# Performance work log

Measured on AMD Instinct MI355X. Metric: run time of the kernel, lower is better.

The kernel has to match this reference:

```python
import jax, jax.numpy as jnp
import numpy as np

N_NODES = 100000
N_EDGES = 600000
NODE_IN = 387
HID = 128
EDGE_DIM = 7


def _p(key, shape, scale=0.02):
    return jax.random.normal(key, shape, dtype=jnp.float32) * scale


def setup_inputs() -> dict:
    key = jax.random.key(0)
    ks = jax.random.split(key, 24)
    x = jax.random.normal(ks[0], (N_NODES, NODE_IN), dtype=jnp.float32)
    edge_index = jax.random.randint(ks[1], (2, N_EDGES), 0, N_NODES, dtype=jnp.int64)
    edge_attr = jax.random.normal(ks[2], (N_EDGES, EDGE_DIM), dtype=jnp.float32)
    return {
        "x": x,
        "edge_index": edge_index,
        "edge_attr": edge_attr,
        # conv1: edge lin (7 -> 387), mlp (387 -> 128 -> 128)
        "e1_w": _p(ks[3], (EDGE_DIM, NODE_IN)), "e1_b": jnp.zeros((NODE_IN,), jnp.float32),
        "m1_w1": _p(ks[4], (NODE_IN, HID)), "m1_b1": jnp.zeros((HID,), jnp.float32),
        "m1_w2": _p(ks[5], (HID, HID)), "m1_b2": jnp.zeros((HID,), jnp.float32),
        # conv2: edge lin (7 -> 128), mlp (128 -> 128 -> 128)
        "e2_w": _p(ks[6], (EDGE_DIM, HID)), "e2_b": jnp.zeros((HID,), jnp.float32),
        "m2_w1": _p(ks[7], (HID, HID)), "m2_b1": jnp.zeros((HID,), jnp.float32),
        "m2_w2": _p(ks[8], (HID, HID)), "m2_b2": jnp.zeros((HID,), jnp.float32),
        # edge_mlp: (2*128+7 -> 128 -> 2); dropout is identity at eval
        "em_w1": _p(ks[9], (2 * HID + EDGE_DIM, HID)), "em_b1": jnp.zeros((HID,), jnp.float32),
        "em_w2": _p(ks[10], (HID, 2)), "em_b2": jnp.zeros((2,), jnp.float32),
    }


def gine_conv(x, src, dst, edge_attr, ew, eb, w1, b1, w2, b2, eps=0.0):
    # message: relu(x_j + Lin(edge_attr)); aggregate sum at destination
    msg = jax.nn.relu(x[src] + edge_attr @ ew + eb)  # [E, D]
    aggr = jax.ops.segment_sum(msg, dst, num_segments=x.shape[0])  # [N, D]
    h = (1.0 + eps) * x + aggr
    return jax.nn.relu(h @ w1 + b1) @ w2 + b2


def reference(x, edge_index, edge_attr,
              e1_w, e1_b, m1_w1, m1_b1, m1_w2, m1_b2,
              e2_w, e2_b, m2_w1, m2_b1, m2_w2, m2_b2,
              em_w1, em_b1, em_w2, em_b2):
    src, dst = edge_index[0], edge_index[1]
    h = gine_conv(x, src, dst, edge_attr, e1_w, e1_b, m1_w1, m1_b1, m1_w2, m1_b2)
    h = jax.nn.relu(h)
    h = gine_conv(h, src, dst, edge_attr, e2_w, e2_b, m2_w1, m2_b1, m2_w2, m2_b2)
    h = jax.nn.relu(h)
    edge_input = jnp.concatenate([h[src], h[dst], edge_attr], axis=1)  # [E, 263]
    return jax.nn.relu(edge_input @ em_w1 + em_b1) @ em_w2 + em_b2  # [E, 2]
```

## Files before the change

kernel.cpp:

```cpp
#include <hip/hip_runtime.h>


using f32x4 = __attribute__((ext_vector_type(4))) float;
using s16x8 = __attribute__((ext_vector_type(8))) short;

#define N_NODES 100000
#define N_EDGES 600000
#define NODE_IN 387
#define KPAD    416
#define HID     128
#define NB_SCAN 391

__device__ __forceinline__ unsigned short f2bf(float f) {
    unsigned u = __float_as_uint(f);
    u += 0x7FFFu + ((u >> 16) & 1u);
    return (unsigned short)(u >> 16);
}

__global__ __launch_bounds__(256) void k_decode(const unsigned* __restrict__ w,
                                                int* __restrict__ s32,
                                                int* __restrict__ d32) {
    __shared__ unsigned long long bs[4];
    __shared__ int is64_s;
    const int t = threadIdx.x;
    unsigned any = 0;
    for (int i = 1 + 2 * t; i < 2048; i += 512) any |= w[i];
    unsigned long long b = __ballot(any != 0);
    if ((t & 63) == 0) bs[t >> 6] = b;
    __syncthreads();
    if (t == 0) is64_s = ((bs[0] | bs[1] | bs[2] | bs[3]) == 0ULL) ? 1 : 0;
    __syncthreads();
    const int is64 = is64_s;
    const int e = blockIdx.x * 256 + t;
    if (e < N_EDGES) {
        if (is64) {
            s32[e] = (int)w[2 * e];
            d32[e] = (int)w[2 * N_EDGES + 2 * e];
        } else {
            s32[e] = (int)w[e];
            d32[e] = (int)w[N_EDGES + e];
        }
    }
}

__global__ __launch_bounds__(256) void k_prep(const float* __restrict__ w1,
                                              const float* __restrict__ w2,
                                              const float* __restrict__ v1,
                                              const float* __restrict__ v2,
                                              const float* __restrict__ ew1,
                                              unsigned short* __restrict__ W1t,
                                              unsigned short* __restrict__ W2t,
                                              unsigned short* __restrict__ V1t,
                                              unsigned short* __restrict__ V2t,
                                              unsigned short* __restrict__ EW1t) {
    int i = blockIdx.x * 256 + threadIdx.x;
    if (i < 128 * KPAD) {
        int c = i / KPAD, k = i - c * KPAD;
        W1t[i] = (k < NODE_IN) ? f2bf(w1[k * HID + c]) : (unsigned short)0;
        return;
    }
    i -= 128 * KPAD;
    if (i < 16384) { int c = i >> 7, k = i & 127; W2t[i] = f2bf(w2[k * HID + c]); return; }
    i -= 16384;
    if (i < 16384) { int c = i >> 7, k = i & 127; V1t[i] = f2bf(v1[k * HID + c]); return; }
    i -= 16384;
    if (i < 16384) { int c = i >> 7, k = i & 127; V2t[i] = f2bf(v2[k * HID + c]); return; }
    i -= 16384;
    if (i < 32768) { int c = i >> 8, k = i & 255; EW1t[i] = f2bf(ew1[k * HID + c]); return; }
}

__global__ __launch_bounds__(256) void k_hist(const int* __restrict__ d32,
                                              int* __restrict__ cnt) {
    const int e = blockIdx.x * 256 + threadIdx.x;
    if (e < N_EDGES) atomicAdd(&cnt[d32[e]], 1);
}

__global__ __launch_bounds__(256) void k_scanA(const int* __restrict__ cnt,
                                               int* __restrict__ bsum) {
    __shared__ int wt[4];
    const int t = threadIdx.x;
    const int i = blockIdx.x * 256 + t;
    int v = (i < N_NODES) ? cnt[i] : 0;
#pragma unroll
    for (int off = 32; off; off >>= 1) v += __shfl_down(v, off);
    if ((t & 63) == 0) wt[t >> 6] = v;
    __syncthreads();
    if (t == 0) bsum[blockIdx.x] = wt[0] + wt[1] + wt[2] + wt[3];
}

__global__ __launch_bounds__(256) void k_scanC(int* __restrict__ cnt,
                                               const int* __restrict__ bsum) {
    __shared__ int wt[4];
    __shared__ int wt2[4];
    __shared__ int sh_bofs;
    const int t = threadIdx.x, b = blockIdx.x;
    int accp = 0;
    for (int i = t; i < NB_SCAN; i += 256) if (i < b) accp += bsum[i];
#pragma unroll
    for (int off = 32; off; off >>= 1) accp += __shfl_down(accp, off);
    if ((t & 63) == 0) wt[t >> 6] = accp;
    __syncthreads();
    if (t == 0) sh_bofs = wt[0] + wt[1] + wt[2] + wt[3];
    const int i = b * 256 + t;
    const int v = (i < N_NODES) ? cnt[i] : 0;
    int inc = v;
    const int lane = t & 63;
#pragma unroll
    for (int off = 1; off < 64; off <<= 1) {
        int u = __shfl_up(inc, off);
        if (lane >= off) inc += u;
    }
    if (lane == 63) wt2[t >> 6] = inc;
    __syncthreads();
    int wbase = 0;
    for (int wI = 0; wI < (t >> 6); ++wI) wbase += wt2[wI];
    if (i < N_NODES) cnt[i] = sh_bofs + wbase + inc - v;
}

__global__ __launch_bounds__(256) void k_scatter(const int* __restrict__ s32,
                                                 const int* __restrict__ d32,
                                                 int* __restrict__ cur,
                                                 int* __restrict__ ss2,
                                                 int* __restrict__ ds2,
                                                 int* __restrict__ ep) {
    const int e = blockIdx.x * 256 + threadIdx.x;
    if (e < N_EDGES) {
        const int d = d32[e];
        const int pos = atomicAdd(&cur[d], 1);
        ss2[pos] = s32[e];
        ds2[pos] = d;
        ep[pos]  = e;
    }
}

#define STAGE_B(dst, srcbase, stride_) do {                                   \
    const int col_ = t >> 1, h_ = t & 1;                                      \
    *(s16x8*)&(dst)[col_ * 40 + h_ * 16] =                                    \
        *(const s16x8*)&(srcbase)[col_ * (stride_) + h_ * 16];                \
    *(s16x8*)&(dst)[col_ * 40 + h_ * 16 + 8] =                                \
        *(const s16x8*)&(srcbase)[col_ * (stride_) + h_ * 16 + 8];            \
} while (0)

__global__ __launch_bounds__(256) void k_edge1(const float* __restrict__ x,
                                               const int* __restrict__ ss2,
                                               const int* __restrict__ ds2,
                                               const int* __restrict__ ep,
                                               const float* __restrict__ ea,
                                               const float* __restrict__ e1w,
                                               const float* __restrict__ e1b,
                                               const unsigned short* __restrict__ W1t,
                                               float* __restrict__ yagg) {
    __shared__ __align__(16) char pool[31488];
    unsigned short* Asm = (unsigned short*)(pool);
    unsigned short* Bsm = (unsigned short*)(pool + 5120);
    float* e1w_s = (float*)(pool + 15360);
    float* e1b_s = (float*)(pool + 27008);
    float* ea_s  = (float*)(pool + 28672);
    int* ss_s    = (int*)(pool + 30720);
    int* dst_s   = (int*)(pool + 30976);
    int* ep_s    = (int*)(pool + 31232);
    float* Csm   = (float*)(pool);

    const int t = threadIdx.x;
    const int e0 = blockIdx.x * 64;

    if (t < 64) ss_s[t] = ss2[e0 + t];
    else if (t < 128) dst_s[t - 64] = ds2[e0 + (t - 64)];
    else if (t < 192) ep_s[t - 128] = ep[e0 + (t - 128)];
    for (int i = t; i < 7 * KPAD; i += 256) {
        int q = i / KPAD, k = i - q * KPAD;
        e1w_s[i] = (k < NODE_IN) ? e1w[q * NODE_IN + k] : 0.f;
    }
    for (int i = t; i < KPAD; i += 256) e1b_s[i] = (i < NODE_IN) ? e1b[i] : 0.f;
    __syncthreads();
    for (int i = t; i < 64 * 7; i += 256) {
        int r = i / 7, q = i - r * 7;
        ea_s[r * 8 + q] = ea[ep_s[r] * 7 + q];
    }
    __syncthreads();

    const int lane = t & 63, wid = t >> 6;
    const int wr = wid >> 1, wc = wid & 1;
    const int r = t >> 2, kc = (t & 3) * 8;
    const int srow = ss_s[r];
    float eav[7];
#pragma unroll
    for (int q = 0; q < 7; ++q) eav[q] = ea_s[r * 8 + q];

    f32x4 acc[2][4];
    const f32x4 zero = {0.f, 0.f, 0.f, 0.f};
#pragma unroll
    for (int mi = 0; mi < 2; ++mi)
#pragma unroll
        for (int ni = 0; ni < 4; ++ni) acc[mi][ni] = zero;

    for (int ks = 0; ks < 13; ++ks) {
        {
            const int kb = ks * 32 + kc;
            s16x8 v;
#pragma unroll
            for (int j = 0; j < 8; ++j) {
                const int k = kb + j;
                float val = 0.f;
                if (k < NODE_IN) {
                    float le = e1b_s[k];
#pragma unroll
                    for (int q = 0; q < 7; ++q) le = fmaf(eav[q], e1w_s[q * KPAD + k], le);
                    val = x[srow * NODE_IN + k] + le;
                    val = fmaxf(val, 0.f);
                }
                v[j] = (short)f2bf(val);
            }
            *(s16x8*)&Asm[r * 40 + kc] = v;
        }
        STAGE_B(Bsm, &W1t[ks * 32], KPAD);
        __syncthreads();
        const int koff = (lane >> 4) * 8;
        const int rA = lane & 15;
        s16x8 a0 = *(const s16x8*)&Asm[(wr * 32 + rA) * 40 + koff];
        s16x8 a1 = *(const s16x8*)&Asm[(wr * 32 + 16 + rA) * 40 + koff];
#pragma unroll
        for (int ni = 0; ni < 4; ++ni) {
            s16x8 b = *(const s16x8*)&Bsm[(wc * 64 + ni * 16 + rA) * 40 + koff];
            acc[0][ni] = __builtin_amdgcn_mfma_f32_16x16x32_bf16(a0, b, acc[0][ni], 0, 0, 0);
            acc[1][ni] = __builtin_amdgcn_mfma_f32_16x16x32_bf16(a1, b, acc[1][ni], 0, 0, 0);
        }
        __syncthreads();
    }
    const int g = lane >> 4;
    const int cb = wc * 64 + (lane & 15);
#pragma unroll
    for (int p = 0; p < 2; ++p) {
        if (wr == p) {
#pragma unroll
            for (int mi = 0; mi < 2; ++mi)
#pragma unroll
                for (int reg = 0; reg < 4; ++reg) {
                    const int row = mi * 16 + g * 4 + reg;
#pragma unroll
                    for (int ni = 0; ni < 4; ++ni)
                        Csm[row * 129 + cb + ni * 16] = acc[mi][ni][reg];
                }
        }
        __syncthreads();
        if (t < 128) {
            const int base = p * 32;
            float s = 0.f;
            int prev = dst_s[base];
            for (int rr = 0; rr < 32; ++rr) {
                const int d = dst_s[base + rr];
                const float v = Csm[rr * 129 + t];
                if (d != prev) { atomicAdd(&yagg[prev * HID + t], s); s = 0.f; prev = d; }
                s += v;
            }
            atomicAdd(&yagg[prev * HID + t], s);
        }
        __syncthreads();
    }
}

__global__ __launch_bounds__(256) void k_node1(const float* __restrict__ x,
                                               const float* __restrict__ yagg,
                                               const unsigned short* __restrict__ W1t,
                                               const unsigned short* __restrict__ W2t,
                                               const float* __restrict__ b1,
                                               const float* __restrict__ b2,
                                               float* __restrict__ r1) {
    __shared__ __align__(16) unsigned short Asm[64 * 40];
    __shared__ __align__(16) unsigned short Bsm[128 * 40];
    __shared__ __align__(16) unsigned short Hsm[64 * 136];
    const int t = threadIdx.x;
    const int i0 = blockIdx.x * 64;
    const int lane = t & 63, wid = t >> 6, wr = wid >> 1, wc = wid & 1;
    const int r = t >> 2, kc = (t & 3) * 8;
    const int rg = i0 + r;
    const bool rvalid = rg < N_NODES;

    f32x4 acc[2][4];
    const f32x4 zero = {0.f, 0.f, 0.f, 0.f};
#pragma unroll
    for (int mi = 0; mi < 2; ++mi)
#pragma unroll
        for (int ni = 0; ni < 4; ++ni) acc[mi][ni] = zero;

    for (int ks = 0; ks < 13; ++ks) {
        {
            const int kb = ks * 32 + kc;
            s16x8 v;
#pragma unroll
            for (int j = 0; j < 8; ++j) {
                const int k = kb + j;
                float val = (rvalid && k < NODE_IN) ? x[rg * NODE_IN + k] : 0.f;
                v[j] = (short)f2bf(val);
            }
            *(s16x8*)&Asm[r * 40 + kc] = v;
        }
        STAGE_B(Bsm, &W1t[ks * 32], KPAD);
        __syncthreads();
        const int koff = (lane >> 4) * 8;
        const int rA = lane & 15;
        s16x8 a0 = *(const s16x8*)&Asm[(wr * 32 + rA) * 40 + koff];
        s16x8 a1 = *(const s16x8*)&Asm[(wr * 32 + 16 + rA) * 40 + koff];
#pragma unroll
        for (int ni = 0; ni < 4; ++ni) {
            s16x8 b = *(const s16x8*)&Bsm[(wc * 64 + ni * 16 + rA) * 40 + koff];
            acc[0][ni] = __builtin_amdgcn_mfma_f32_16x16x32_bf16(a0, b, acc[0][ni], 0, 0, 0);
            acc[1][ni] = __builtin_amdgcn_mfma_f32_16x16x32_bf16(a1, b, acc[1][ni], 0, 0, 0);
        }
        __syncthreads();
    }
    const int jb = wc * 64 + (lane & 15);
#pragma unroll
    for (int mi = 0; mi < 2; ++mi) {
#pragma unroll
        for (int reg = 0; reg < 4; ++reg) {
            const int rloc = wr * 32 + mi * 16 + (lane >> 4) * 4 + reg;
            const int rowg = i0 + rloc;
#pragma unroll
            for (int ni = 0; ni < 4; ++ni) {
                const int j = jb + ni * 16;
                float v = acc[mi][ni][reg];
                if (rowg < N_NODES) {
                    v += yagg[rowg * HID + j] + b1[j];
                    v = fmaxf(v, 0.f);
                } else v = 0.f;
                Hsm[rloc * 136 + j] = f2bf(v);
            }
        }
    }
    __syncthreads();
    f32x4 acc2[2][4];
#pragma unroll
    for (int mi = 0; mi < 2; ++mi)
#pragma unroll
        for (int ni = 0; ni < 4; ++ni) acc2[mi][ni] = zero;

    for (int ks = 0; ks < 4; ++ks) {
        STAGE_B(Bsm, &W2t[ks * 32], HID);
        __syncthreads();
        const int koff = (lane >> 4) * 8;
        const int rA = lane & 15;
        s16x8 a0 = *(const s16x8*)&Hsm[(wr * 32 + rA) * 136 + ks * 32 + koff];
        s16x8 a1 = *(const s16x8*)&Hsm[(wr * 32 + 16 + rA) * 136 + ks * 32 + koff];
#pragma unroll
        for (int ni = 0; ni < 4; ++ni) {
            s16x8 b = *(const s16x8*)&Bsm[(wc * 64 + ni * 16 + rA) * 40 + koff];
            acc2[0][ni] = __builtin_amdgcn_mfma_f32_16x16x32_bf16(a0, b, acc2[0][ni], 0, 0, 0);
            acc2[1][ni] = __builtin_amdgcn_mfma_f32_16x16x32_bf16(a1, b, acc2[1][ni], 0, 0, 0);
        }
        __syncthreads();
    }
#pragma unroll
    for (int mi = 0; mi < 2; ++mi) {
#pragma unroll
        for (int reg = 0; reg < 4; ++reg) {
            const int rloc = wr * 32 + mi * 16 + (lane >> 4) * 4 + reg;
            const int rowg = i0 + rloc;
            if (rowg < N_NODES) {
#pragma unroll
                for (int ni = 0; ni < 4; ++ni) {
                    const int j = jb + ni * 16;
                    float v = acc2[mi][ni][reg] + b2[j];
                    r1[rowg * HID + j] = fmaxf(v, 0.f);
                }
            }
        }
    }
}

__global__ __launch_bounds__(256) void k_edge2(const float* __restrict__ r1,
                                               const int* __restrict__ ss2,
                                               const int* __restrict__ ds2,
                                               const int* __restrict__ ep,
                                               const float* __restrict__ ea,
                                               const float* __restrict__ e2w,
                                               const float* __restrict__ e2b,
                                               float* __restrict__ agg2) {
    __shared__ float w_s[7 * HID];
    __shared__ float b_s[HID];
    __shared__ float Csm[64 * 129];
    __shared__ int ss_s[64];
    __shared__ int ds_s[64];
    __shared__ int pe_s[64];
    const int t = threadIdx.x;
    const int e0 = blockIdx.x * 64;
    for (int i = t; i < 7 * HID; i += 256) w_s[i] = e2w[i];
    if (t < HID) b_s[t] = e2b[t];
    if (t < 64) ss_s[t] = ss2[e0 + t];
    else if (t < 128) ds_s[t - 64] = ds2[e0 + (t - 64)];
    else if (t < 192) pe_s[t - 128] = ep[e0 + (t - 128)];
    __syncthreads();

    const int r = t >> 2, c0 = (t & 3) * 32;
    const int s = ss_s[r];
    const int pe = pe_s[r];
    float eav[7];
#pragma unroll
    for (int q = 0; q < 7; ++q) eav[q] = ea[pe * 7 + q];
    const f32x4* rp = (const f32x4*)&r1[s * HID + c0];
#pragma unroll
    for (int u = 0; u < 8; ++u) {
        f32x4 v4 = rp[u];
#pragma unroll
        for (int j = 0; j < 4; ++j) {
            const int c = c0 + u * 4 + j;
            float v = v4[j] + b_s[c];
#pragma unroll
            for (int q = 0; q < 7; ++q) v = fmaf(eav[q], w_s[q * HID + c], v);
            Csm[r * 129 + c] = fmaxf(v, 0.f);
        }
    }
    __syncthreads();
    if (t < 128) {
        float ssum = 0.f;
        int prev = ds_s[0];
        for (int rr = 0; rr < 64; ++rr) {
            const int d = ds_s[rr];
            const float v = Csm[rr * 129 + t];
            if (d != prev) { atomicAdd(&agg2[prev * HID + t], ssum); ssum = 0.f; prev = d; }
            ssum += v;
        }
        atomicAdd(&agg2[prev * HID + t], ssum);
    }
}

__global__ __launch_bounds__(256) void k_node2(const float* __restrict__ r1,
                                               const float* __restrict__ agg2,
                                               const unsigned short* __restrict__ V1t,
                                               const unsigned short* __restrict__ V2t,
                                               const float* __restrict__ b1,
                                               const float* __restrict__ b2,
                                               unsigned short* __restrict__ r2) {
    __shared__ __align__(16) unsigned short Asm[64 * 40];
    __shared__ __align__(16) unsigned short Bsm[128 * 40];
    __shared__ __align__(16) unsigned short Hsm[64 * 136];
    const int t = threadIdx.x;
    const int i0 = blockIdx.x * 64;
    const int lane = t & 63, wid = t >> 6, wr = wid >> 1, wc = wid & 1;
    const int r = t >> 2, kc = (t & 3) * 8;
    const int rg = i0 + r;
    const bool rvalid = rg < N_NODES;

    f32x4 acc[2][4];
    const f32x4 zero = {0.f, 0.f, 0.f, 0.f};
#pragma unroll
    for (int mi = 0; mi < 2; ++mi)
#pragma unroll
        for (int ni = 0; ni < 4; ++ni) acc[mi][ni] = zero;

    for (int ks = 0; ks < 4; ++ks) {
        {
            const int kb = ks * 32 + kc;
            s16x8 v;
            if (rvalid) {
                const f32x4* pa = (const f32x4*)&r1[rg * HID + kb];
                const f32x4* pb = (const f32x4*)&agg2[rg * HID + kb];
                f32x4 u0 = pa[0], u1 = pa[1], w0 = pb[0], w1 = pb[1];
#pragma unroll
                for (int j = 0; j < 4; ++j) v[j] = (short)f2bf(u0[j] + w0[j]);
#pragma unroll
                for (int j = 0; j < 4; ++j) v[4 + j] = (short)f2bf(u1[j] + w1[j]);
            } else {
#pragma unroll
                for (int j = 0; j < 8; ++j) v[j] = 0;
            }
            *(s16x8*)&Asm[r * 40 + kc] = v;
        }
        STAGE_B(Bsm, &V1t[ks * 32], HID);
        __syncthreads();
        const int koff = (lane >> 4) * 8;
        const int rA = lane & 15;
        s16x8 a0 = *(const s16x8*)&Asm[(wr * 32 + rA) * 40 + koff];
        s16x8 a1 = *(const s16x8*)&Asm[(wr * 32 + 16 + rA) * 40 + koff];
#pragma unroll
        for (int ni = 0; ni < 4; ++ni) {
            s16x8 b = *(const s16x8*)&Bsm[(wc * 64 + ni * 16 + rA) * 40 + koff];
            acc[0][ni] = __builtin_amdgcn_mfma_f32_16x16x32_bf16(a0, b, acc[0][ni], 0, 0, 0);
            acc[1][ni] = __builtin_amdgcn_mfma_f32_16x16x32_bf16(a1, b, acc[1][ni], 0, 0, 0);
        }
        __syncthreads();
    }
    const int jb = wc * 64 + (lane & 15);
#pragma unroll
    for (int mi = 0; mi < 2; ++mi) {
#pragma unroll
        for (int reg = 0; reg < 4; ++reg) {
            const int rloc = wr * 32 + mi * 16 + (lane >> 4) * 4 + reg;
            const int rowg = i0 + rloc;
#pragma unroll
            for (int ni = 0; ni < 4; ++ni) {
                const int j = jb + ni * 16;
                float v = acc[mi][ni][reg];
                if (rowg < N_NODES) {
                    v += b1[j];
                    v = fmaxf(v, 0.f);
                } else v = 0.f;
                Hsm[rloc * 136 + j] = f2bf(v);
            }
        }
    }
    __syncthreads();
    f32x4 acc2[2][4];
#pragma unroll
    for (int mi = 0; mi < 2; ++mi)
#pragma unroll
        for (int ni = 0; ni < 4; ++ni) acc2[mi][ni] = zero;

    for (int ks = 0; ks < 4; ++ks) {
        STAGE_B(Bsm, &V2t[ks * 32], HID);
        __syncthreads();
        const int koff = (lane >> 4) * 8;
        const int rA = lane & 15;
        s16x8 a0 = *(const s16x8*)&Hsm[(wr * 32 + rA) * 136 + ks * 32 + koff];
        s16x8 a1 = *(const s16x8*)&Hsm[(wr * 32 + 16 + rA) * 136 + ks * 32 + koff];
#pragma unroll
        for (int ni = 0; ni < 4; ++ni) {
            s16x8 b = *(const s16x8*)&Bsm[(wc * 64 + ni * 16 + rA) * 40 + koff];
            acc2[0][ni] = __builtin_amdgcn_mfma_f32_16x16x32_bf16(a0, b, acc2[0][ni], 0, 0, 0);
            acc2[1][ni] = __builtin_amdgcn_mfma_f32_16x16x32_bf16(a1, b, acc2[1][ni], 0, 0, 0);
        }
        __syncthreads();
    }
#pragma unroll
    for (int mi = 0; mi < 2; ++mi) {
#pragma unroll
        for (int reg = 0; reg < 4; ++reg) {
            const int rloc = wr * 32 + mi * 16 + (lane >> 4) * 4 + reg;
            const int rowg = i0 + rloc;
            if (rowg < N_NODES) {
#pragma unroll
                for (int ni = 0; ni < 4; ++ni) {
                    const int j = jb + ni * 16;
                    float v = acc2[mi][ni][reg] + b2[j];
                    r2[rowg * HID + j] = f2bf(fmaxf(v, 0.f));
                }
            }
        }
    }
}

__global__ __launch_bounds__(256) void k_head(const unsigned short* __restrict__ r2,
                                              const int* __restrict__ srcp,
                                              const int* __restrict__ dstp,
                                              const float* __restrict__ ea,
                                              const unsigned short* __restrict__ EW1t,
                                              const float* __restrict__ emw1,
                                              const float* __restrict__ emb1,
                                              const float* __restrict__ emw2,
                                              const float* __restrict__ emb2,
                                              float* __restrict__ out) {
    __shared__ __align__(16) unsigned short Asm[64 * 40];
    __shared__ __align__(16) unsigned short Bsm[128 * 40];
    __shared__ float Hsm[64 * 129];
    __shared__ float ew_ea[7 * HID];
    __shared__ float eb1_s[HID];
    __shared__ float w2_s[256];
    __shared__ float b2_s[2];
    __shared__ float ea_s[64 * 8];
    __shared__ int src_s[64];
    __shared__ int dst_s[64];
    __shared__ float red[512];
    const int t = threadIdx.x;
    const int e0 = blockIdx.x * 64;

    for (int i = t; i < 7 * HID; i += 256) ew_ea[i] = emw1[256 * HID + i];
    if (t < HID) eb1_s[t] = emb1[t];
    if (t < 256) w2_s[t] = emw2[t];
    if (t < 2) b2_s[t] = emb2[t];
    for (int i = t; i < 64 * 7; i += 256) {
        int r = i / 7, q = i - r * 7;
        ea_s[r * 8 + q] = ea[(e0 + r) * 7 + q];
    }
    if (t < 64) src_s[t] = srcp[e0 + t];
    else if (t < 128) dst_s[t - 64] = dstp[e0 + (t - 64)];
    __syncthreads();

    const int lane = t & 63, wid = t >> 6, wr = wid >> 1, wc = wid & 1;
    const int r = t >> 2, kc = (t & 3) * 8;

    f32x4 acc[2][4];
    const f32x4 zero = {0.f, 0.f, 0.f, 0.f};
#pragma unroll
    for (int mi = 0; mi < 2; ++mi)
#pragma unroll
        for (int ni = 0; ni < 4; ++ni) acc[mi][ni] = zero;

    for (int ks = 0; ks < 8; ++ks) {
        {
            const int k = ks * 32 + kc;
            const unsigned short* p = (k < HID) ? &r2[src_s[r] * HID + k]
                                                : &r2[dst_s[r] * HID + (k - HID)];
            *(s16x8*)&Asm[r * 40 + kc] = *(const s16x8*)p;
        }
        STAGE_B(Bsm, &EW1t[ks * 32], 256);
        __syncthreads();
        const int koff = (lane >> 4) * 8;
        const int rA = lane & 15;
        s16x8 a0 = *(const s16x8*)&Asm[(wr * 32 + rA) * 40 + koff];
        s16x8 a1 = *(const s16x8*)&Asm[(wr * 32 + 16 + rA) * 40 + koff];
#pragma unroll
        for (int ni = 0; ni < 4; ++ni) {
            s16x8 b = *(const s16x8*)&Bsm[(wc * 64 + ni * 16 + rA) * 40 + koff];
            acc[0][ni] = __builtin_amdgcn_mfma_f32_16x16x32_bf16(a0, b, acc[0][ni], 0, 0, 0);
            acc[1][ni] = __builtin_amdgcn_mfma_f32_16x16x32_bf16(a1, b, acc[1][ni], 0, 0, 0);
        }
        __syncthreads();
    }
    const int jb = wc * 64 + (lane & 15);
#pragma unroll
    for (int mi = 0; mi < 2; ++mi) {
#pragma unroll
        for (int reg = 0; reg < 4; ++reg) {
            const int rloc = wr * 32 + mi * 16 + (lane >> 4) * 4 + reg;
#pragma unroll
            for (int ni = 0; ni < 4; ++ni) {
                const int j = jb + ni * 16;
                float v = acc[mi][ni][reg] + eb1_s[j];
#pragma unroll
                for (int q = 0; q < 7; ++q)
                    v = fmaf(ea_s[rloc * 8 + q], ew_ea[q * HID + j], v);
                Hsm[rloc * 129 + j] = fmaxf(v, 0.f);
            }
        }
    }
    __syncthreads();
    {
        const int e = t & 63, p = t >> 6;
        const float* hb = &Hsm[e * 129 + p * 32];
        float s0 = 0.f, s1 = 0.f;
#pragma unroll
        for (int j = 0; j < 32; ++j) {
            const float h = hb[j];
            s0 = fmaf(h, w2_s[(p * 32 + j) * 2], s0);
            s1 = fmaf(h, w2_s[(p * 32 + j) * 2 + 1], s1);
        }
        red[(e * 4 + p) * 2] = s0;
        red[(e * 4 + p) * 2 + 1] = s1;
    }
    __syncthreads();
    if (t < 64) {
        float o0 = b2_s[0], o1 = b2_s[1];
#pragma unroll
        for (int p = 0; p < 4; ++p) {
            o0 += red[(t * 4 + p) * 2];
            o1 += red[(t * 4 + p) * 2 + 1];
        }
        out[(e0 + t) * 2] = o0;
        out[(e0 + t) * 2 + 1] = o1;
    }
}

extern "C" void kernel_launch(void* const* d_in, const int* in_sizes, int n_in,
                              void* d_out, int out_size, void* d_ws, size_t ws_size,
                              hipStream_t stream) {
    (void)in_sizes; (void)n_in; (void)out_size; (void)ws_size;
    const float* x    = (const float*)d_in[0];
    const unsigned* eidx = (const unsigned*)d_in[1];
    const float* ea   = (const float*)d_in[2];
    const float* e1w  = (const float*)d_in[3];
    const float* e1b  = (const float*)d_in[4];
    const float* m1w1 = (const float*)d_in[5];
    const float* m1b1 = (const float*)d_in[6];
    const float* m1w2 = (const float*)d_in[7];
    const float* m1b2 = (const float*)d_in[8];
    const float* e2w  = (const float*)d_in[9];
    const float* e2b  = (const float*)d_in[10];
    const float* m2w1 = (const float*)d_in[11];
    const float* m2b1 = (const float*)d_in[12];
    const float* m2w2 = (const float*)d_in[13];
    const float* m2b2 = (const float*)d_in[14];
    const float* emw1 = (const float*)d_in[15];
    const float* emb1 = (const float*)d_in[16];
    const float* emw2 = (const float*)d_in[17];
    const float* emb2 = (const float*)d_in[18];
    float* out = (float*)d_out;

    char* ws = (char*)d_ws;
    float* yagg = (float*)(ws + 0);
    float* r1   = (float*)(ws + 51200000);
    unsigned short* r2   = (unsigned short*)(ws + 102400000);
    unsigned short* W1t  = (unsigned short*)(ws + 128000000);
    unsigned short* W2t  = (unsigned short*)(ws + 128106496);
    unsigned short* V1t  = (unsigned short*)(ws + 128139264);
    unsigned short* V2t  = (unsigned short*)(ws + 128172032);
    unsigned short* EW1t = (unsigned short*)(ws + 128204800);
    int* s32  = (int*)(ws + 128270336);
    int* d32  = (int*)(ws + 130670336);
    int* ss2  = (int*)(ws + 133070336);
    int* ds2  = (int*)(ws + 135470336);
    int* ep   = (int*)(ws + 137870336);
    int* cnt  = (int*)(ws + 140270336);
    int* bsum = (int*)(ws + 140670720);

    hipMemsetAsync(yagg, 0, (size_t)N_NODES * HID * 4, stream);
    hipMemsetAsync(cnt, 0, (size_t)N_NODES * 4, stream);
    k_decode<<<2344, 256, 0, stream>>>(eidx, s32, d32);
    k_prep<<<528, 256, 0, stream>>>(m1w1, m1w2, m2w1, m2w2, emw1, W1t, W2t, V1t, V2t, EW1t);
    k_hist<<<2344, 256, 0, stream>>>(d32, cnt);
    k_scanA<<<NB_SCAN, 256, 0, stream>>>(cnt, bsum);
    k_scanC<<<NB_SCAN, 256, 0, stream>>>(cnt, bsum);
    k_scatter<<<2344, 256, 0, stream>>>(s32, d32, cnt, ss2, ds2, ep);
    k_edge1<<<N_EDGES / 64, 256, 0, stream>>>(x, ss2, ds2, ep, ea, e1w, e1b, W1t, yagg);
    k_node1<<<(N_NODES + 63) / 64, 256, 0, stream>>>(x, yagg, W1t, W2t, m1b1, m1b2, r1);
    hipMemsetAsync(yagg, 0, (size_t)N_NODES * HID * 4, stream);
    k_edge2<<<N_EDGES / 64, 256, 0, stream>>>(r1, ss2, ds2, ep, ea, e2w, e2b, yagg);
    k_node2<<<(N_NODES + 63) / 64, 256, 0, stream>>>(r1, yagg, V1t, V2t, m2b1, m2b2, r2);
    k_head<<<N_EDGES / 64, 256, 0, stream>>>(r2, s32, d32, ea, EW1t, emw1, emb1, emw2, emb2, out);
}
```

Measured before the change: 1.107 ms.

## Pre-cast node features to padded bf16 and permute edge attrs in scatter

A new kernel converts x once into a padded bf16 array, so edge1 and node1 gather half the bytes with aligned vector loads and no bounds checks. Edge1 also prefetches the next x slice in its k-loop. Edge attributes are copied in sorted order during scatter, which removes the ep indirection and the dependent gathers in edge1 and edge2. The layer-1 output r1 is stored as bf16 to shrink traffic in edge2 and node2. The cost is an extra cast pass over x, plus extra rounding because x and r1 are now rounded to bf16 before the edge-linear term is added.

```diff
diff --git a/kernel.cpp b/kernel.cpp
--- a/kernel.cpp
+++ b/kernel.cpp
@@ -15,6 +15,9 @@
     unsigned u = __float_as_uint(f);
     u += 0x7FFFu + ((u >> 16) & 1u);
     return (unsigned short)(u >> 16);
+}
+__device__ __forceinline__ float bf2f(short h) {
+    return __uint_as_float(((unsigned)(unsigned short)h) << 16);
 }
 
 __global__ __launch_bounds__(256) void k_decode(const unsigned* __restrict__ w,
@@ -69,6 +72,20 @@
     if (i < 32768) { int c = i >> 8, k = i & 255; EW1t[i] = f2bf(ew1[k * HID + c]); return; }
 }
 
+__global__ __launch_bounds__(256) void k_castx(const float* __restrict__ x,
+                                               unsigned short* __restrict__ xbf) {
+    const int g = blockIdx.x * 256 + threadIdx.x;
+    if (g >= N_NODES * 52) return;
+    const int row = g / 52, c0 = (g - row * 52) * 8;
+    s16x8 v;
+#pragma unroll
+    for (int j = 0; j < 8; ++j) {
+        const int c = c0 + j;
+        v[j] = (c < NODE_IN) ? (short)f2bf(x[row * NODE_IN + c]) : (short)0;
+    }
+    *(s16x8*)&xbf[row * KPAD + c0] = v;
+}
+
 __global__ __launch_bounds__(256) void k_hist(const int* __restrict__ d32,
                                               int* __restrict__ cnt) {
     const int e = blockIdx.x * 256 + threadIdx.x;
@@ -119,17 +136,20 @@
 
 __global__ __launch_bounds__(256) void k_scatter(const int* __restrict__ s32,
                                                  const int* __restrict__ d32,
+                                                 const float* __restrict__ ea,
                                                  int* __restrict__ cur,
                                                  int* __restrict__ ss2,
                                                  int* __restrict__ ds2,
-                                                 int* __restrict__ ep) {
+                                                 float* __restrict__ eas) {
     const int e = blockIdx.x * 256 + threadIdx.x;
     if (e < N_EDGES) {
         const int d = d32[e];
         const int pos = atomicAdd(&cur[d], 1);
         ss2[pos] = s32[e];
         ds2[pos] = d;
-        ep[pos]  = e;
+#pragma unroll
+        for (int q = 0; q < 7; ++q) eas[pos * 8 + q] = ea[e * 7 + q];
+        eas[pos * 8 + 7] = 0.f;
     }
 }
 
@@ -141,16 +161,15 @@
         *(const s16x8*)&(srcbase)[col_ * (stride_) + h_ * 16 + 8];            \
 } while (0)
 
-__global__ __launch_bounds__(256) void k_edge1(const float* __restrict__ x,
+__global__ __launch_bounds__(256) void k_edge1(const unsigned short* __restrict__ xbf,
                                                const int* __restrict__ ss2,
                                                const int* __restrict__ ds2,
-                                               const int* __restrict__ ep,
-                                               const float* __restrict__ ea,
+                                               const float* __restrict__ eas,
                                                const float* __restrict__ e1w,
                                                const float* __restrict__ e1b,
                                                const unsigned short* __restrict__ W1t,
                                                float* __restrict__ yagg) {
-    __shared__ __align__(16) char pool[31488];
+    __shared__ __align__(16) char pool[31232];
     unsigned short* Asm = (unsigned short*)(pool);
     unsigned short* Bsm = (unsigned short*)(pool + 5120);
     float* e1w_s = (float*)(pool + 15360);
@@ -158,7 +177,6 @@
     float* ea_s  = (float*)(pool + 28672);
     int* ss_s    = (int*)(pool + 30720);
     int* dst_s   = (int*)(pool + 30976);
-    int* ep_s    = (int*)(pool + 31232);
     float* Csm   = (float*)(pool);
 
     const int t = threadIdx.x;
@@ -166,17 +184,12 @@
 
     if (t < 64) ss_s[t] = ss2[e0 + t];
     else if (t < 128) dst_s[t - 64] = ds2[e0 + (t - 64)];
-    else if (t < 192) ep_s[t - 128] = ep[e0 + (t - 128)];
     for (int i = t; i < 7 * KPAD; i += 256) {
         int q = i / KPAD, k = i - q * KPAD;
         e1w_s[i] = (k < NODE_IN) ? e1w[q * NODE_IN + k] : 0.f;
     }
     for (int i = t; i < KPAD; i += 256) e1b_s[i] = (i < NODE_IN) ? e1b[i] : 0.f;
-    __syncthreads();
-    for (int i = t; i < 64 * 7; i += 256) {
-        int r = i / 7, q = i - r * 7;
-        ea_s[r * 8 + q] = ea[ep_s[r] * 7 + q];
-    }
+    for (int i = t; i < 512; i += 256) ea_s[i] = eas[e0 * 8 + i];
     __syncthreads();
 
     const int lane = t & 63, wid = t >> 6;
@@ -194,22 +207,20 @@
 #pragma unroll
         for (int ni = 0; ni < 4; ++ni) acc[mi][ni] = zero;
 
+    s16x8 xa_n = *(const s16x8*)&xbf[srow * KPAD + kc];
     for (int ks = 0; ks < 13; ++ks) {
+        const s16x8 xa = xa_n;
+        if (ks < 12) xa_n = *(const s16x8*)&xbf[srow * KPAD + (ks + 1) * 32 + kc];
         {
             const int kb = ks * 32 + kc;
             s16x8 v;
 #pragma unroll
             for (int j = 0; j < 8; ++j) {
                 const int k = kb + j;
-                float val = 0.f;
-                if (k < NODE_IN) {
-                    float le = e1b_s[k];
-#pragma unroll
-                    for (int q = 0; q < 7; ++q) le = fmaf(eav[q], e1w_s[q * KPAD + k], le);
-                    val = x[srow * NODE_IN + k] + le;
-                    val = fmaxf(val, 0.f);
-                }
-                v[j] = (short)f2bf(val);
+                float le = e1b_s[k];
+#pragma unroll
+                for (int q = 0; q < 7; ++q) le = fmaf(eav[q], e1w_s[q * KPAD + k], le);
+                v[j] = (short)f2bf(fmaxf(bf2f(xa[j]) + le, 0.f));
             }
             *(s16x8*)&Asm[r * 40 + kc] = v;
         }
@@ -259,13 +270,13 @@
     }
 }
 
-__global__ __launch_bounds__(256) void k_node1(const float* __restrict__ x,
+__global__ __launch_bounds__(256) void k_node1(const unsigned short* __restrict__ xbf,
                                                const float* __restrict__ yagg,
                                                const unsigned short* __restrict__ W1t,
                                                const unsigned short* __restrict__ W2t,
                                                const float* __restrict__ b1,
                                                const float* __restrict__ b2,
-                                               float* __restrict__ r1) {
+                                               unsigned short* __restrict__ r1b) {
     __shared__ __align__(16) unsigned short Asm[64 * 40];
     __shared__ __align__(16) unsigned short Bsm[128 * 40];
     __shared__ __align__(16) unsigned short Hsm[64 * 136];
@@ -285,13 +296,11 @@
 
     for (int ks = 0; ks < 13; ++ks) {
         {
-            const int kb = ks * 32 + kc;
             s16x8 v;
-#pragma unroll
-            for (int j = 0; j < 8; ++j) {
-                const int k = kb + j;
-                float val = (rvalid && k < NODE_IN) ? x[rg * NODE_IN + k] : 0.f;
-                v[j] = (short)f2bf(val);
+            if (rvalid) v = *(const s16x8*)&xbf[rg * KPAD + ks * 32 + kc];
+            else {
+#pragma unroll
+                for (int j = 0; j < 8; ++j) v[j] = 0;
             }
             *(s16x8*)&Asm[r * 40 + kc] = v;
         }
@@ -361,50 +370,48 @@
                 for (int ni = 0; ni < 4; ++ni) {
                     const int j = jb + ni * 16;
                     float v = acc2[mi][ni][reg] + b2[j];
-                    r1[rowg * HID + j] = fmaxf(v, 0.f);
+                    r1b[rowg * HID + j] = f2bf(fmaxf(v, 0.f));
                 }
             }
         }
     }
 }
 
-__global__ __launch_bounds__(256) void k_edge2(const float* __restrict__ r1,
+__global__ __launch_bounds__(256) void k_edge2(const unsigned short* __restrict__ r1b,
                                                const int* __restrict__ ss2,
                                                const int* __restrict__ ds2,
-                                               const int* __restrict__ ep,
-                                               const float* __restrict__ ea,
+                                               const float* __restrict__ eas,
                                                const float* __restrict__ e2w,
                                                const float* __restrict__ e2b,
                                                float* __restrict__ agg2) {
     __shared__ float w_s[7 * HID];
     __shared__ float b_s[HID];
     __shared__ float Csm[64 * 129];
+    __shared__ float ea_s[64 * 8];
     __shared__ int ss_s[64];
     __shared__ int ds_s[64];
-    __shared__ int pe_s[64];
     const int t = threadIdx.x;
     const int e0 = blockIdx.x * 64;
     for (int i = t; i < 7 * HID; i += 256) w_s[i] = e2w[i];
     if (t < HID) b_s[t] = e2b[t];
     if (t < 64) ss_s[t] = ss2[e0 + t];
     else if (t < 128) ds_s[t - 64] = ds2[e0 + (t - 64)];
-    else if (t < 192) pe_s[t - 128] = ep[e0 + (t - 128)];
+    for (int i = t; i < 512; i += 256) ea_s[i] = eas[e0 * 8 + i];
     __syncthreads();
 
     const int r = t >> 2, c0 = (t & 3) * 32;
     const int s = ss_s[r];
-    const int pe = pe_s[r];
     float eav[7];
 #pragma unroll
-    for (int q = 0; q < 7; ++q) eav[q] = ea[pe * 7 + q];
-    const f32x4* rp = (const f32x4*)&r1[s * HID + c0];
-#pragma unroll
-    for (int u = 0; u < 8; ++u) {
-        f32x4 v4 = rp[u];
-#pragma unroll
-        for (int j = 0; j < 4; ++j) {
-            const int c = c0 + u * 4 + j;
-            float v = v4[j] + b_s[c];
+    for (int q = 0; q < 7; ++q) eav[q] = ea_s[r * 8 + q];
+    const s16x8* rp = (const s16x8*)&r1b[s * HID + c0];
+#pragma unroll
+    for (int u = 0; u < 4; ++u) {
+        s16x8 hv = rp[u];
+#pragma unroll
+        for (int j = 0; j < 8; ++j) {
+            const int c = c0 + u * 8 + j;
+            float v = bf2f(hv[j]) + b_s[c];
 #pragma unroll
             for (int q = 0; q < 7; ++q) v = fmaf(eav[q], w_s[q * HID + c], v);
             Csm[r * 129 + c] = fmaxf(v, 0.f);
@@ -424,7 +431,7 @@
     }
 }
 
-__global__ __launch_bounds__(256) void k_node2(const float* __restrict__ r1,
+__global__ __launch_bounds__(256) void k_node2(const unsigned short* __restrict__ r1b,
                                                const float* __restrict__ agg2,
                                                const unsigned short* __restrict__ V1t,
                                                const unsigned short* __restrict__ V2t,
@@ -453,13 +460,13 @@
             const int kb = ks * 32 + kc;
             s16x8 v;
             if (rvalid) {
-                const f32x4* pa = (const f32x4*)&r1[rg * HID + kb];
+                const s16x8 ra = *(const s16x8*)&r1b[rg * HID + kb];
                 const f32x4* pb = (const f32x4*)&agg2[rg * HID + kb];
-                f32x4 u0 = pa[0], u1 = pa[1], w0 = pb[0], w1 = pb[1];
-#pragma unroll
-                for (int j = 0; j < 4; ++j) v[j] = (short)f2bf(u0[j] + w0[j]);
-#pragma unroll
-                for (int j = 0; j < 4; ++j) v[4 + j] = (short)f2bf(u1[j] + w1[j]);
+                f32x4 w0 = pb[0], w1 = pb[1];
+#pragma unroll
+                for (int j = 0; j < 4; ++j) v[j] = (short)f2bf(bf2f(ra[j]) + w0[j]);
+#pragma unroll
+                for (int j = 0; j < 4; ++j) v[4 + j] = (short)f2bf(bf2f(ra[4 + j]) + w1[j]);
             } else {
 #pragma unroll
                 for (int j = 0; j < 8; ++j) v[j] = 0;
@@ -677,33 +684,35 @@
 
     char* ws = (char*)d_ws;
     float* yagg = (float*)(ws + 0);
-    float* r1   = (float*)(ws + 51200000);
-    unsigned short* r2   = (unsigned short*)(ws + 102400000);
-    unsigned short* W1t  = (unsigned short*)(ws + 128000000);
-    unsigned short* W2t  = (unsigned short*)(ws + 128106496);
-    unsigned short* V1t  = (unsigned short*)(ws + 128139264);
-    unsigned short* V2t  = (unsigned short*)(ws + 128172032);
-    unsigned short* EW1t = (unsigned short*)(ws + 128204800);
-    int* s32  = (int*)(ws + 128270336);
-    int* d32  = (int*)(ws + 130670336);
-    int* ss2  = (int*)(ws + 133070336);
-    int* ds2  = (int*)(ws + 135470336);
-    int* ep   = (int*)(ws + 137870336);
-    int* cnt  = (int*)(ws + 140270336);
-    int* bsum = (int*)(ws + 140670720);
+    unsigned short* r1b = (unsigned short*)(ws + 51200000);
+    unsigned short* r2  = (unsigned short*)(ws + 76800000);
+    float* eas          = (float*)(ws + 76800000);
+    unsigned short* xbf = (unsigned short*)(ws + 102400000);
+    unsigned short* W1t  = (unsigned short*)(ws + 185600000);
+    unsigned short* W2t  = (unsigned short*)(ws + 185706496);
+    unsigned short* V1t  = (unsigned short*)(ws + 185739264);
+    unsigned short* V2t  = (unsigned short*)(ws + 185772032);
+    unsigned short* EW1t = (unsigned short*)(ws + 185804800);
+    int* s32  = (int*)(ws + 185870336);
+    int* d32  = (int*)(ws + 188270336);
+    int* ss2  = (int*)(ws + 190670336);
+    int* ds2  = (int*)(ws + 193070336);
+    int* cnt  = (int*)(ws + 195470336);
+    int* bsum = (int*)(ws + 195870336);
 
     hipMemsetAsync(yagg, 0, (size_t)N_NODES * HID * 4, stream);
     hipMemsetAsync(cnt, 0, (size_t)N_NODES * 4, stream);
     k_decode<<<2344, 256, 0, stream>>>(eidx, s32, d32);
     k_prep<<<528, 256, 0, stream>>>(m1w1, m1w2, m2w1, m2w2, emw1, W1t, W2t, V1t, V2t, EW1t);
+    k_castx<<<(N_NODES * 52 + 255) / 256, 256, 0, stream>>>(x, xbf);
     k_hist<<<2344, 256, 0, stream>>>(d32, cnt);
     k_scanA<<<NB_SCAN, 256, 0, stream>>>(cnt, bsum);
     k_scanC<<<NB_SCAN, 256, 0, stream>>>(cnt, bsum);
-    k_scatter<<<2344, 256, 0, stream>>>(s32, d32, cnt, ss2, ds2, ep);
-    k_edge1<<<N_EDGES / 64, 256, 0, stream>>>(x, ss2, ds2, ep, ea, e1w, e1b, W1t, yagg);
-    k_node1<<<(N_NODES + 63) / 64, 256, 0, stream>>>(x, yagg, W1t, W2t, m1b1, m1b2, r1);
+    k_scatter<<<2344, 256, 0, stream>>>(s32, d32, ea, cnt, ss2, ds2, eas);
+    k_edge1<<<N_EDGES / 64, 256, 0, stream>>>(xbf, ss2, ds2, eas, e1w, e1b, W1t, yagg);
+    k_node1<<<(N_NODES + 63) / 64, 256, 0, stream>>>(xbf, yagg, W1t, W2t, m1b1, m1b2, r1b);
     hipMemsetAsync(yagg, 0, (size_t)N_NODES * HID * 4, stream);
-    k_edge2<<<N_EDGES / 64, 256, 0, stream>>>(r1, ss2, ds2, ep, ea, e2w, e2b, yagg);
-    k_node2<<<(N_NODES + 63) / 64, 256, 0, stream>>>(r1, yagg, V1t, V2t, m2b1, m2b2, r2);
+    k_edge2<<<N_EDGES / 64, 256, 0, stream>>>(r1b, ss2, ds2, eas, e2w, e2b, yagg);
+    k_node2<<<(N_NODES + 63) / 64, 256, 0, stream>>>(r1b, yagg, V1t, V2t, m2b1, m2b2, r2);
     k_head<<<N_EDGES / 64, 256, 0, stream>>>(r2, s32, d32, ea, EW1t, emw1, emb1, emw2, emb2, out);
 }
```

Result: faster. 1.076 ms (-2.8%).
